# Performance work log

Hardware: AMD Instinct MI355X
Metric: run time of the kernel (lower is better)

## Reference

```python
import jax, jax.numpy as jnp
import numpy as np

B, N, D = 256, 128, 512
NUM_TYPES, NUM_STATS = 6, 8
W_TYPE, W_STATS, W_CORR = 1.0, 1.0, 0.5
LN_EPS = 1e-5


def setup_inputs() -> dict:
    key = jax.random.key(0)
    ks = jax.random.split(key, 20)
    s = 1.0 / np.sqrt(D)
    inp = {
        "column_embeddings": jax.random.normal(ks[0], (B, N, D), jnp.float32),
        "masked_columns": jax.random.bernoulli(ks[1], 0.15, (B, N)),
        "type_targets": jax.random.randint(ks[2], (N,), 0, NUM_TYPES),
        "column_statistics": jax.random.normal(ks[3], (B, N, NUM_STATS), jnp.float32),
        "column_correlations": jnp.tanh(jax.random.normal(ks[4], (B, N, N), jnp.float32)),
        # type head: Linear(D,D) -> GELU -> LayerNorm -> Linear(D,NUM_TYPES)
        "t_W1": jax.random.normal(ks[5], (D, D), jnp.float32) * s,
        "t_b1": jnp.zeros((D,), jnp.float32),
        "t_g": jnp.ones((D,), jnp.float32),
        "t_beta": jnp.zeros((D,), jnp.float32),
        "t_W2": jax.random.normal(ks[6], (D, NUM_TYPES), jnp.float32) * s,
        "t_b2": jnp.zeros((NUM_TYPES,), jnp.float32),
        # stats head
        "s_W1": jax.random.normal(ks[7], (D, D), jnp.float32) * s,
        "s_b1": jnp.zeros((D,), jnp.float32),
        "s_g": jnp.ones((D,), jnp.float32),
        "s_beta": jnp.zeros((D,), jnp.float32),
        "s_W2": jax.random.normal(ks[8], (D, NUM_STATS), jnp.float32) * s,
        "s_b2": jnp.zeros((NUM_STATS,), jnp.float32),
        # bilinear correlation: x_i^T W x_j + b
        "c_W": jax.random.normal(ks[9], (D, D), jnp.float32) * s,
        "c_b": jnp.zeros((), jnp.float32),
    }
    return inp


def _mlp_head(x, W1, b1, g, beta, W2, b2):
    h = jax.nn.gelu(x @ W1 + b1, approximate=False)
    mu = h.mean(-1, keepdims=True)
    var = ((h - mu) ** 2).mean(-1, keepdims=True)
    h = (h - mu) * jax.lax.rsqrt(var + LN_EPS) * g + beta
    return h @ W2 + b2


def _forward(column_embeddings, masked_columns, type_targets,
             column_statistics, column_correlations,
             t_W1, t_b1, t_g, t_beta, t_W2, t_b2,
             s_W1, s_b1, s_g, s_beta, s_W2, s_b2,
             c_W, c_b):
    e = column_embeddings  # [B,N,D]
    type_logits = _mlp_head(e, t_W1, t_b1, t_g, t_beta, t_W2, t_b2)   # [B,N,T]
    stats_preds = _mlp_head(e, s_W1, s_b1, s_g, s_beta, s_W2, s_b2)   # [B,N,S]

    # batched bilinear correlation: tanh(e_i W e_j + b), diag forced to 1
    u = jnp.einsum('bnd,de->bne', e, c_W)            # [B,N,D]
    corr = jnp.tanh(jnp.einsum('bne,bme->bnm', u, e) + c_b)  # [B,N,N]
    eye = jnp.eye(e.shape[1], dtype=corr.dtype)
    corr = corr * (1.0 - eye) + eye

    m = masked_columns.astype(jnp.float32)           # [B,N]
    n_masked = jnp.maximum(m.sum(), 1.0)

    # type loss: masked-mean cross entropy; targets broadcast over batch
    logp = jax.nn.log_softmax(type_logits, axis=-1)
    tgt = jnp.broadcast_to(type_targets[None, :], m.shape)
    ce = -jnp.take_along_axis(logp, tgt[..., None], axis=-1)[..., 0]  # [B,N]
    type_loss = (ce * m).sum() / n_masked

    # stats loss: masked-mean MSE over [B,N,S]
    se = (stats_preds - column_statistics) ** 2
    stats_loss = (se * m[..., None]).sum() / (n_masked * se.shape[-1])

    # correlation loss: mask_expanded = m_i | m_j
    me = jnp.maximum(m[:, :, None], m[:, None, :])   # [B,N,N]
    n_me = jnp.maximum(me.sum(), 1.0)
    ce2 = (corr - column_correlations) ** 2
    correlation_loss = (ce2 * me).sum() / n_me

    total = W_TYPE * type_loss + W_STATS * stats_loss + W_CORR * correlation_loss
    return total


def reference(column_embeddings, masked_columns, type_targets,
              column_statistics, column_correlations,
              t_W1, t_b1, t_g, t_beta, t_W2, t_b2,
              s_W1, s_b1, s_g, s_beta, s_W2, s_b2,
              c_W, c_b):
    return _forward(column_embeddings, masked_columns, type_targets,
                    column_statistics, column_correlations,
                    t_W1, t_b1, t_g, t_beta, t_W2, t_b2,
                    s_W1, s_b1, s_g, s_beta, s_W2, s_b2,
                    c_W, c_b)
```

## Files before the change

kernel.cpp:

```cpp
#include <hip/hip_runtime.h>
#include <math.h>

#define Bx 256
#define Nx 128
#define Dx 512
#define Mx (Bx * Nx)
#define NTYPES 6
#define NSTATS 8
#define LN_EPS 1e-5f
#define CAP 8192

typedef __attribute__((ext_vector_type(8))) short frag8;
typedef __attribute__((ext_vector_type(4))) float f32x4;

__device__ __forceinline__ unsigned short f2bf(float f) {
    unsigned u = __float_as_uint(f);
    u += 0x7fff + ((u >> 16) & 1);
    return (unsigned short)(u >> 16);
}
__device__ __forceinline__ float bf2f(unsigned short s) {
    return __uint_as_float((unsigned)s << 16);
}

#define ASYNC16(g, l) __builtin_amdgcn_global_load_lds(                      \
    (const __attribute__((address_space(1))) void*)(g),                      \
    (__attribute__((address_space(3))) void*)(l), 16, 0, 0)

#define EB_OFF    0ULL
#define U_OFF     33554432ULL
#define EC_OFF    67108864ULL
#define HC_OFF    75497472ULL
#define WT_OFF    92274688ULL
#define WTC_OFF   93323264ULL
#define LIST_OFF  93847552ULL
#define CNTS_OFF  93978624ULL
#define PACC_OFF  93979648ULL
#define PCORR_OFF 93981696ULL
#define ACC_OFF   93982720ULL

__global__ void k_init(int* cntp) {
    if (threadIdx.x == 0) *cntp = 0;
}

__global__ void k_mask_build(const int* __restrict__ m, int* __restrict__ list,
                             int* __restrict__ cnts, int* cntp) {
    const int b = blockIdx.x;
    const int t = threadIdx.x;
    const int r = b * Nx + t;
    const int v = (m[r] != 0) ? 1 : 0;
    const unsigned long long bal = __ballot(v);
    const int wid = t >> 6, lane = t & 63;
    __shared__ int wcnt[2];
    __shared__ int base;
    if (lane == 0) wcnt[wid] = __popcll(bal);
    __syncthreads();
    const int cnt = wcnt[0] + wcnt[1];
    if (t == 0) {
        base = atomicAdd(cntp, cnt);
        cnts[b] = cnt;
    }
    __syncthreads();
    if (v) {
        const int rank = __popcll(bal & ((1ULL << lane) - 1)) + (wid ? wcnt[0] : 0);
        list[base + rank] = r;
    }
}

__global__ void k_convE(const float* __restrict__ x, unsigned short* __restrict__ y) {
    const int i = blockIdx.x * blockDim.x + threadIdx.x;
    const float4 a = ((const float4*)x)[2 * i];
    const float4 b = ((const float4*)x)[2 * i + 1];
    unsigned short u[8] = {f2bf(a.x), f2bf(a.y), f2bf(a.z), f2bf(a.w),
                           f2bf(b.x), f2bf(b.y), f2bf(b.z), f2bf(b.w)};
    ((uint4*)y)[i] = *(const uint4*)u;
}

__global__ void k_convW(const float* __restrict__ W, unsigned short* __restrict__ Wt) {
    const int i = blockIdx.x * blockDim.x + threadIdx.x;
    const int n = i >> 9, k = i & 511;
    Wt[i] = f2bf(W[k * Dx + n]);
}

__global__ void k_gather(const unsigned short* __restrict__ Eb,
                         const int* __restrict__ list, const int* __restrict__ cntp,
                         unsigned short* __restrict__ Ec) {
    const int idx = blockIdx.x;
    const int cnt = min(*cntp, CAP);
    if (idx >= cnt) return;
    const int r = list[idx];
    ((unsigned*)(Ec + (size_t)idx * Dx))[threadIdx.x] =
        ((const unsigned*)(Eb + (size_t)r * Dx))[threadIdx.x];
}

template <int MODE>
__global__ __launch_bounds__(256) void k_gemm_mfma(
    const unsigned short* __restrict__ A,
    const unsigned short* __restrict__ Bt,
    const float* __restrict__ bias0, const float* __restrict__ bias1,
    unsigned short* __restrict__ Cout, int ldc, const int* __restrict__ cntp) {
    const int row0 = blockIdx.y * 128;
    if (MODE == 0) {
        if (row0 >= min(*cntp, CAP)) return;
    }
    __shared__ unsigned short As[128 * 32];
    __shared__ unsigned short Bs[128 * 32];
    const int t = threadIdx.x;
    const int col0 = blockIdx.x * 128;
    const int w = t >> 6, l = t & 63;
    const int wr = (w >> 1) * 64, wc = (w & 1) * 64;
    const int quad = l >> 4, mr = l & 15;

    const unsigned short* Ag0 = A + (size_t)(row0 + (t >> 2)) * Dx + (t & 3) * 8;
    const unsigned short* Ag1 = Ag0 + (size_t)64 * Dx;
    const unsigned short* Bg0 = Bt + (size_t)(col0 + (t >> 2)) * Dx + (t & 3) * 8;
    const unsigned short* Bg1 = Bg0 + (size_t)64 * Dx;
    unsigned short* Al0 = As + t * 8;
    unsigned short* Al1 = As + (t + 256) * 8;
    unsigned short* Bl0 = Bs + t * 8;
    unsigned short* Bl1 = Bs + (t + 256) * 8;

    f32x4 acc[4][4] = {};

    for (int k0 = 0; k0 < Dx; k0 += 32) {
        __syncthreads();
        ASYNC16(Ag0 + k0, Al0);
        ASYNC16(Ag1 + k0, Al1);
        ASYNC16(Bg0 + k0, Bl0);
        ASYNC16(Bg1 + k0, Bl1);
        __syncthreads();
        frag8 a[4], b[4];
#pragma unroll
        for (int i = 0; i < 4; ++i)
            a[i] = *(const frag8*)&As[(wr + i * 16 + mr) * 32 + quad * 8];
#pragma unroll
        for (int j = 0; j < 4; ++j)
            b[j] = *(const frag8*)&Bs[(wc + j * 16 + mr) * 32 + quad * 8];
#pragma unroll
        for (int i = 0; i < 4; ++i)
#pragma unroll
            for (int j = 0; j < 4; ++j)
                acc[i][j] = __builtin_amdgcn_mfma_f32_16x16x32_bf16(
                    a[i], b[j], acc[i][j], 0, 0, 0);
    }

#pragma unroll
    for (int i = 0; i < 4; ++i)
#pragma unroll
        for (int j = 0; j < 4; ++j)
#pragma unroll
            for (int r = 0; r < 4; ++r) {
                const int row = row0 + wr + i * 16 + quad * 4 + r;
                const int col = col0 + wc + j * 16 + mr;
                float v = acc[i][j][r];
                if (MODE == 0) {
                    v += (col < 512) ? bias0[col] : bias1[col - 512];
                    v = 0.5f * v * (1.0f + erff(v * 0.70710678118654752f));
                }
                Cout[(size_t)row * ldc + col] = f2bf(v);
            }
}

__global__ __launch_bounds__(256) void k_head2(
    const unsigned short* __restrict__ Hc,
    const float* __restrict__ tg, const float* __restrict__ tbeta,
    const float* __restrict__ tW2, const float* __restrict__ tb2,
    const float* __restrict__ sg, const float* __restrict__ sbeta,
    const float* __restrict__ sW2, const float* __restrict__ sb2,
    const int* __restrict__ list, const int* __restrict__ cntp,
    const int* __restrict__ tgt, const float* __restrict__ stats,
    float* __restrict__ pacc) {
    const int t = threadIdx.x, w = t >> 6, lane = t & 63;
    const int cnt = min(*cntp, CAP);
    float ce_acc = 0.0f, sse_acc = 0.0f;

    for (int idx = blockIdx.x * 4 + w; idx < cnt; idx += gridDim.x * 4) {
        const int r = list[idx];
        const uint4 ut = ((const uint4*)(Hc + (size_t)idx * 1024))[lane];
        const uint4 us = ((const uint4*)(Hc + (size_t)idx * 1024 + 512))[lane];
        float a[8], b8[8];
        {
            const unsigned uu[4] = {ut.x, ut.y, ut.z, ut.w};
            const unsigned vv[4] = {us.x, us.y, us.z, us.w};
#pragma unroll
            for (int j = 0; j < 4; ++j) {
                a[2 * j]      = bf2f((unsigned short)(uu[j] & 0xffff));
                a[2 * j + 1]  = bf2f((unsigned short)(uu[j] >> 16));
                b8[2 * j]     = bf2f((unsigned short)(vv[j] & 0xffff));
                b8[2 * j + 1] = bf2f((unsigned short)(vv[j] >> 16));
            }
        }
        float st = 0, qt = 0, ss = 0, qs = 0;
#pragma unroll
        for (int j = 0; j < 8; ++j) {
            st += a[j]; qt += a[j] * a[j];
            ss += b8[j]; qs += b8[j] * b8[j];
        }
#pragma unroll
        for (int off = 32; off > 0; off >>= 1) {
            st += __shfl_xor(st, off); qt += __shfl_xor(qt, off);
            ss += __shfl_xor(ss, off); qs += __shfl_xor(qs, off);
        }
        const float mt = st * (1.0f / Dx);
        const float rt = rsqrtf(qt * (1.0f / Dx) - mt * mt + LN_EPS);
        const float ms = ss * (1.0f / Dx);
        const float rs = rsqrtf(qs * (1.0f / Dx) - ms * ms + LN_EPS);

        const int c0 = lane * 8;
        float tp[6] = {}, sp[8] = {};
#pragma unroll
        for (int j = 0; j < 8; ++j) {
            const int c = c0 + j;
            const float nt = (a[j] - mt) * rt * tg[c] + tbeta[c];
#pragma unroll
            for (int k = 0; k < 6; ++k) tp[k] += nt * tW2[c * 6 + k];
            const float ns = (b8[j] - ms) * rs * sg[c] + sbeta[c];
#pragma unroll
            for (int k = 0; k < 8; ++k) sp[k] += ns * sW2[c * 8 + k];
        }
#pragma unroll
        for (int k = 0; k < 6; ++k)
#pragma unroll
            for (int off = 32; off > 0; off >>= 1) tp[k] += __shfl_down(tp[k], off);
#pragma unroll
        for (int k = 0; k < 8; ++k)
#pragma unroll
            for (int off = 32; off > 0; off >>= 1) sp[k] += __shfl_down(sp[k], off);

        if (lane == 0) {
            float lg[6];
#pragma unroll
            for (int k = 0; k < 6; ++k) lg[k] = tp[k] + tb2[k];
            float mx = lg[0];
#pragma unroll
            for (int k = 1; k < 6; ++k) mx = fmaxf(mx, lg[k]);
            float se = 0.0f;
#pragma unroll
            for (int k = 0; k < 6; ++k) se += expf(lg[k] - mx);
            ce_acc += -(lg[tgt[r & (Nx - 1)]] - mx - logf(se));
            float sse = 0.0f;
#pragma unroll
            for (int k = 0; k < 8; ++k) {
                const float d = sp[k] + sb2[k] - stats[(size_t)r * NSTATS + k];
                sse += d * d;
            }
            sse_acc += sse;
        }
    }
    __shared__ float red[4][2];
    if (lane == 0) { red[w][0] = ce_acc; red[w][1] = sse_acc; }
    __syncthreads();
    if (t == 0) {
        pacc[2 * blockIdx.x]     = red[0][0] + red[1][0] + red[2][0] + red[3][0];
        pacc[2 * blockIdx.x + 1] = red[0][1] + red[1][1] + red[2][1] + red[3][1];
    }
}

__global__ __launch_bounds__(256) void k_corr_mfma(
    const unsigned short* __restrict__ U,
    const unsigned short* __restrict__ E,
    const float* __restrict__ Ct,
    const int* __restrict__ m,
    const float* __restrict__ cbp,
    float* __restrict__ pcorr) {
    __shared__ unsigned short As[128 * 32];
    __shared__ unsigned short Bs[128 * 32];
    __shared__ float mloc[128];
    __shared__ float red[4];
    const int b = blockIdx.x;
    const int t = threadIdx.x;
    const int w = t >> 6, l = t & 63;
    const int wr = (w >> 1) * 64, wc = (w & 1) * 64;
    const int quad = l >> 4, mr = l & 15;

    if (t < 128) mloc[t] = (m[b * Nx + t] != 0) ? 1.0f : 0.0f;

    const unsigned short* Ub = U + (size_t)b * Nx * Dx;
    const unsigned short* Eb = E + (size_t)b * Nx * Dx;
    const unsigned short* Ag0 = Ub + (size_t)(t >> 2) * Dx + (t & 3) * 8;
    const unsigned short* Ag1 = Ag0 + (size_t)64 * Dx;
    const unsigned short* Bg0 = Eb + (size_t)(t >> 2) * Dx + (t & 3) * 8;
    const unsigned short* Bg1 = Bg0 + (size_t)64 * Dx;
    unsigned short* Al0 = As + t * 8;
    unsigned short* Al1 = As + (t + 256) * 8;
    unsigned short* Bl0 = Bs + t * 8;
    unsigned short* Bl1 = Bs + (t + 256) * 8;

    f32x4 acc_r[4][4] = {};

    for (int k0 = 0; k0 < Dx; k0 += 32) {
        __syncthreads();
        ASYNC16(Ag0 + k0, Al0);
        ASYNC16(Ag1 + k0, Al1);
        ASYNC16(Bg0 + k0, Bl0);
        ASYNC16(Bg1 + k0, Bl1);
        __syncthreads();
        frag8 a[4], bfr[4];
#pragma unroll
        for (int i = 0; i < 4; ++i)
            a[i] = *(const frag8*)&As[(wr + i * 16 + mr) * 32 + quad * 8];
#pragma unroll
        for (int j = 0; j < 4; ++j)
            bfr[j] = *(const frag8*)&Bs[(wc + j * 16 + mr) * 32 + quad * 8];
#pragma unroll
        for (int i = 0; i < 4; ++i)
#pragma unroll
            for (int j = 0; j < 4; ++j)
                acc_r[i][j] = __builtin_amdgcn_mfma_f32_16x16x32_bf16(
                    a[i], bfr[j], acc_r[i][j], 0, 0, 0);
    }

    const float cb = cbp[0];
    float lsum = 0.0f;
#pragma unroll
    for (int i = 0; i < 4; ++i)
#pragma unroll
        for (int j = 0; j < 4; ++j)
#pragma unroll
            for (int r = 0; r < 4; ++r) {
                const int row = wr + i * 16 + quad * 4 + r;
                const int col = wc + j * 16 + mr;
                float c = (row == col) ? 1.0f : tanhf(acc_r[i][j][r] + cb);
                const float me = fmaxf(mloc[row], mloc[col]);
                const float d = c - Ct[((size_t)b * Nx + row) * Nx + col];
                lsum += me * d * d;
            }
#pragma unroll
    for (int off = 32; off > 0; off >>= 1) lsum += __shfl_down(lsum, off);
    if (l == 0) red[w] = lsum;
    __syncthreads();
    if (t == 0) pcorr[b] = red[0] + red[1] + red[2] + red[3];
}

__global__ __launch_bounds__(256) void k_final(
    const float* __restrict__ pacc, const float* __restrict__ pcorr,
    const int* __restrict__ cnts, const int* __restrict__ cntp,
    float* __restrict__ out) {
    const int t = threadIdx.x, w = t >> 6, lane = t & 63;
    float ce = pacc[2 * t], sse = pacc[2 * t + 1], co = pcorr[t];
    const int c = cnts[t];
    float me = (float)(Nx * Nx) - (float)((Nx - c) * (Nx - c));
#pragma unroll
    for (int off = 32; off > 0; off >>= 1) {
        ce += __shfl_down(ce, off);
        sse += __shfl_down(sse, off);
        co += __shfl_down(co, off);
        me += __shfl_down(me, off);
    }
    __shared__ float red[4][4];
    if (lane == 0) {
        red[w][0] = ce; red[w][1] = sse; red[w][2] = co; red[w][3] = me;
    }
    __syncthreads();
    if (t == 0) {
        const float CE = red[0][0] + red[1][0] + red[2][0] + red[3][0];
        const float SSE = red[0][1] + red[1][1] + red[2][1] + red[3][1];
        const float CO = red[0][2] + red[1][2] + red[2][2] + red[3][2];
        const float ME = red[0][3] + red[1][3] + red[2][3] + red[3][3];
        const float nm = fmaxf((float)*cntp, 1.0f);
        const float nme = fmaxf(ME, 1.0f);
        out[0] = CE / nm + SSE / (nm * (float)NSTATS) + 0.5f * CO / nme;
    }
}

extern "C" void kernel_launch(void* const* d_in, const int* in_sizes, int n_in,
                              void* d_out, int out_size, void* d_ws, size_t ws_size,
                              hipStream_t stream) {
    const float* e      = (const float*)d_in[0];
    const int*   mcols  = (const int*)d_in[1];
    const int*   ttgt   = (const int*)d_in[2];
    const float* stats  = (const float*)d_in[3];
    const float* corrT  = (const float*)d_in[4];
    const float* tW1    = (const float*)d_in[5];
    const float* tb1    = (const float*)d_in[6];
    const float* tg     = (const float*)d_in[7];
    const float* tbeta  = (const float*)d_in[8];
    const float* tW2    = (const float*)d_in[9];
    const float* tb2    = (const float*)d_in[10];
    const float* sW1    = (const float*)d_in[11];
    const float* sb1    = (const float*)d_in[12];
    const float* sg     = (const float*)d_in[13];
    const float* sbeta  = (const float*)d_in[14];
    const float* sW2    = (const float*)d_in[15];
    const float* sb2    = (const float*)d_in[16];
    const float* cW     = (const float*)d_in[17];
    const float* cb     = (const float*)d_in[18];
    float* out = (float*)d_out;

    char* ws = (char*)d_ws;
    unsigned short* Eb    = (unsigned short*)(ws + EB_OFF);
    unsigned short* U     = (unsigned short*)(ws + U_OFF);
    unsigned short* Ec    = (unsigned short*)(ws + EC_OFF);
    unsigned short* Hc    = (unsigned short*)(ws + HC_OFF);
    unsigned short* Wtcmb = (unsigned short*)(ws + WT_OFF);
    unsigned short* Wtc   = (unsigned short*)(ws + WTC_OFF);
    int*   list  = (int*)(ws + LIST_OFF);
    int*   cnts  = (int*)(ws + CNTS_OFF);
    float* pacc  = (float*)(ws + PACC_OFF);
    float* pcorr = (float*)(ws + PCORR_OFF);
    int*   cntp  = (int*)(ws + ACC_OFF);

    k_init<<<1, 64, 0, stream>>>(cntp);
    k_mask_build<<<Bx, Nx, 0, stream>>>(mcols, list, cnts, cntp);
    k_convE<<<Mx * Dx / 8 / 256, 256, 0, stream>>>(e, Eb);
    k_convW<<<Dx * Dx / 256, 256, 0, stream>>>(tW1, Wtcmb);
    k_convW<<<Dx * Dx / 256, 256, 0, stream>>>(sW1, Wtcmb + 512 * 512);
    k_convW<<<Dx * Dx / 256, 256, 0, stream>>>(cW, Wtc);
    k_gather<<<CAP, 256, 0, stream>>>(Eb, list, cntp, Ec);

    k_gemm_mfma<0><<<dim3(8, CAP / 128), 256, 0, stream>>>(
        Ec, Wtcmb, tb1, sb1, Hc, 1024, cntp);
    k_head2<<<256, 256, 0, stream>>>(Hc, tg, tbeta, tW2, tb2, sg, sbeta, sW2, sb2,
                                     list, cntp, ttgt, stats, pacc);

    k_gemm_mfma<1><<<dim3(4, 256), 256, 0, stream>>>(
        Eb, Wtc, nullptr, nullptr, U, 512, nullptr);
    k_corr_mfma<<<Bx, 256, 0, stream>>>(U, Eb, corrT, mcols, cb, pcorr);

    k_final<<<1, 256, 0, stream>>>(pacc, pcorr, cnts, cntp, out);
}
```

Before: 256.2 us.

## Fuse bilinear U-GEMM into correlation kernel and merge conversion/gather kernels

The correlation kernel now computes U = E·Wc in 128-column chunks itself, stages each chunk as bf16 in shared memory and multiplies it by E^T, so the 32 MB U intermediate is never written or read from global memory. The embedding conversion and masked-row gather are merged into one kernel that uses a per-row position map, and the three weight transposes plus the counter reset are merged into one launch. This removes several launches and a large round trip through global memory. In exchange, the fused kernel loads E and Wc fragments straight from global memory without LDS tiling and runs only 256 blocks, so it leans on cache hits and may keep fewer MFMA units busy.

```diff
diff --git a/kernel.cpp b/kernel.cpp
--- a/kernel.cpp
+++ b/kernel.cpp
@@ -27,23 +27,34 @@
     (__attribute__((address_space(3))) void*)(l), 16, 0, 0)
 
 #define EB_OFF    0ULL
-#define U_OFF     33554432ULL
-#define EC_OFF    67108864ULL
-#define HC_OFF    75497472ULL
-#define WT_OFF    92274688ULL
-#define WTC_OFF   93323264ULL
-#define LIST_OFF  93847552ULL
-#define CNTS_OFF  93978624ULL
-#define PACC_OFF  93979648ULL
-#define PCORR_OFF 93981696ULL
-#define ACC_OFF   93982720ULL
-
-__global__ void k_init(int* cntp) {
-    if (threadIdx.x == 0) *cntp = 0;
+#define EC_OFF    33554432ULL
+#define HC_OFF    41943040ULL
+#define WT_OFF    58720256ULL
+#define WTC_OFF   59768832ULL
+#define LIST_OFF  60293120ULL
+#define POS_OFF   60424192ULL
+#define CNTS_OFF  60555264ULL
+#define PACC_OFF  60556288ULL
+#define PCORR_OFF 60558336ULL
+#define CNTP_OFF  60559360ULL
+
+__global__ void k_convW_all(const float* __restrict__ W0, const float* __restrict__ W1,
+                            const float* __restrict__ W2,
+                            unsigned short* __restrict__ T0,
+                            unsigned short* __restrict__ T1,
+                            unsigned short* __restrict__ T2, int* cntp) {
+    if (blockIdx.x == 0 && threadIdx.x == 0) *cntp = 0;
+    const int mid = blockIdx.x >> 10;
+    const int i = ((blockIdx.x & 1023) << 8) + threadIdx.x;
+    const int n = i >> 9, k = i & 511;
+    const float* W = (mid == 0) ? W0 : (mid == 1) ? W1 : W2;
+    unsigned short* T = (mid == 0) ? T0 : (mid == 1) ? T1 : T2;
+    T[i] = f2bf(W[k * Dx + n]);
 }
 
 __global__ void k_mask_build(const int* __restrict__ m, int* __restrict__ list,
-                             int* __restrict__ cnts, int* cntp) {
+                             int* __restrict__ pos, int* __restrict__ cnts,
+                             int* cntp) {
     const int b = blockIdx.x;
     const int t = threadIdx.x;
     const int r = b * Nx + t;
@@ -60,54 +71,44 @@
         cnts[b] = cnt;
     }
     __syncthreads();
+    int p = -1;
     if (v) {
         const int rank = __popcll(bal & ((1ULL << lane) - 1)) + (wid ? wcnt[0] : 0);
-        list[base + rank] = r;
-    }
-}
-
-__global__ void k_convE(const float* __restrict__ x, unsigned short* __restrict__ y) {
-    const int i = blockIdx.x * blockDim.x + threadIdx.x;
-    const float4 a = ((const float4*)x)[2 * i];
-    const float4 b = ((const float4*)x)[2 * i + 1];
+        p = base + rank;
+        if (p < CAP) list[p] = r;
+    }
+    pos[r] = (p < CAP) ? p : -1;
+}
+
+__global__ __launch_bounds__(256) void k_convE_gather(
+    const float* __restrict__ e, const int* __restrict__ pos,
+    unsigned short* __restrict__ Eb, unsigned short* __restrict__ Ec) {
+    const int r = blockIdx.x * 4 + (threadIdx.x >> 6);
+    const int lane = threadIdx.x & 63;
+    const float4* src = (const float4*)(e + (size_t)r * Dx);
+    const float4 a = src[lane * 2];
+    const float4 b = src[lane * 2 + 1];
     unsigned short u[8] = {f2bf(a.x), f2bf(a.y), f2bf(a.z), f2bf(a.w),
                            f2bf(b.x), f2bf(b.y), f2bf(b.z), f2bf(b.w)};
-    ((uint4*)y)[i] = *(const uint4*)u;
-}
-
-__global__ void k_convW(const float* __restrict__ W, unsigned short* __restrict__ Wt) {
-    const int i = blockIdx.x * blockDim.x + threadIdx.x;
-    const int n = i >> 9, k = i & 511;
-    Wt[i] = f2bf(W[k * Dx + n]);
-}
-
-__global__ void k_gather(const unsigned short* __restrict__ Eb,
-                         const int* __restrict__ list, const int* __restrict__ cntp,
-                         unsigned short* __restrict__ Ec) {
-    const int idx = blockIdx.x;
-    const int cnt = min(*cntp, CAP);
-    if (idx >= cnt) return;
-    const int r = list[idx];
-    ((unsigned*)(Ec + (size_t)idx * Dx))[threadIdx.x] =
-        ((const unsigned*)(Eb + (size_t)r * Dx))[threadIdx.x];
-}
-
-template <int MODE>
-__global__ __launch_bounds__(256) void k_gemm_mfma(
+    const uint4 v = *(const uint4*)u;
+    ((uint4*)(Eb + (size_t)r * Dx))[lane] = v;
+    const int p = pos[r];
+    if (p >= 0) ((uint4*)(Ec + (size_t)p * Dx))[lane] = v;
+}
+
+__global__ __launch_bounds__(256) void k_gemm_head(
     const unsigned short* __restrict__ A,
     const unsigned short* __restrict__ Bt,
     const float* __restrict__ bias0, const float* __restrict__ bias1,
-    unsigned short* __restrict__ Cout, int ldc, const int* __restrict__ cntp) {
+    unsigned short* __restrict__ Cout, const int* __restrict__ cntp) {
     const int row0 = blockIdx.y * 128;
-    if (MODE == 0) {
-        if (row0 >= min(*cntp, CAP)) return;
-    }
+    if (row0 >= min(*cntp, CAP)) return;
     __shared__ unsigned short As[128 * 32];
     __shared__ unsigned short Bs[128 * 32];
     const int t = threadIdx.x;
     const int col0 = blockIdx.x * 128;
     const int w = t >> 6, l = t & 63;
-    const int wr = (w >> 1) * 64, wc = (w & 1) * 64;
+    const int wr = (w >> 1) * 64, wcol = (w & 1) * 64;
     const int quad = l >> 4, mr = l & 15;
 
     const unsigned short* Ag0 = A + (size_t)(row0 + (t >> 2)) * Dx + (t & 3) * 8;
@@ -120,7 +121,6 @@
     unsigned short* Bl1 = Bs + (t + 256) * 8;
 
     f32x4 acc[4][4] = {};
-
     for (int k0 = 0; k0 < Dx; k0 += 32) {
         __syncthreads();
         ASYNC16(Ag0 + k0, Al0);
@@ -134,7 +134,7 @@
             a[i] = *(const frag8*)&As[(wr + i * 16 + mr) * 32 + quad * 8];
 #pragma unroll
         for (int j = 0; j < 4; ++j)
-            b[j] = *(const frag8*)&Bs[(wc + j * 16 + mr) * 32 + quad * 8];
+            b[j] = *(const frag8*)&Bs[(wcol + j * 16 + mr) * 32 + quad * 8];
 #pragma unroll
         for (int i = 0; i < 4; ++i)
 #pragma unroll
@@ -142,7 +142,6 @@
                 acc[i][j] = __builtin_amdgcn_mfma_f32_16x16x32_bf16(
                     a[i], b[j], acc[i][j], 0, 0, 0);
     }
-
 #pragma unroll
     for (int i = 0; i < 4; ++i)
 #pragma unroll
@@ -150,13 +149,11 @@
 #pragma unroll
             for (int r = 0; r < 4; ++r) {
                 const int row = row0 + wr + i * 16 + quad * 4 + r;
-                const int col = col0 + wc + j * 16 + mr;
+                const int col = col0 + wcol + j * 16 + mr;
                 float v = acc[i][j][r];
-                if (MODE == 0) {
-                    v += (col < 512) ? bias0[col] : bias1[col - 512];
-                    v = 0.5f * v * (1.0f + erff(v * 0.70710678118654752f));
-                }
-                Cout[(size_t)row * ldc + col] = f2bf(v);
+                v += (col < 512) ? bias0[col] : bias1[col - 512];
+                v = 0.5f * v * (1.0f + erff(v * 0.70710678118654752f));
+                Cout[(size_t)row * 1024 + col] = f2bf(v);
             }
 }
 
@@ -255,58 +252,67 @@
     }
 }
 
-__global__ __launch_bounds__(256) void k_corr_mfma(
-    const unsigned short* __restrict__ U,
-    const unsigned short* __restrict__ E,
+__global__ __launch_bounds__(256) void k_corr_fused(
+    const unsigned short* __restrict__ Eb,
+    const unsigned short* __restrict__ Wc,
     const float* __restrict__ Ct,
     const int* __restrict__ m,
     const float* __restrict__ cbp,
     float* __restrict__ pcorr) {
-    __shared__ unsigned short As[128 * 32];
-    __shared__ unsigned short Bs[128 * 32];
+    __shared__ unsigned short Ub[128][136];
     __shared__ float mloc[128];
     __shared__ float red[4];
     const int b = blockIdx.x;
     const int t = threadIdx.x;
     const int w = t >> 6, l = t & 63;
-    const int wr = (w >> 1) * 64, wc = (w & 1) * 64;
+    const int wr = (w >> 1) * 64, wcol = (w & 1) * 64;
     const int quad = l >> 4, mr = l & 15;
-
     if (t < 128) mloc[t] = (m[b * Nx + t] != 0) ? 1.0f : 0.0f;
-
-    const unsigned short* Ub = U + (size_t)b * Nx * Dx;
-    const unsigned short* Eb = E + (size_t)b * Nx * Dx;
-    const unsigned short* Ag0 = Ub + (size_t)(t >> 2) * Dx + (t & 3) * 8;
-    const unsigned short* Ag1 = Ag0 + (size_t)64 * Dx;
-    const unsigned short* Bg0 = Eb + (size_t)(t >> 2) * Dx + (t & 3) * 8;
-    const unsigned short* Bg1 = Bg0 + (size_t)64 * Dx;
-    unsigned short* Al0 = As + t * 8;
-    unsigned short* Al1 = As + (t + 256) * 8;
-    unsigned short* Bl0 = Bs + t * 8;
-    unsigned short* Bl1 = Bs + (t + 256) * 8;
-
-    f32x4 acc_r[4][4] = {};
-
-    for (int k0 = 0; k0 < Dx; k0 += 32) {
+    const unsigned short* E = Eb + (size_t)b * Nx * Dx;
+
+    f32x4 S[4][4] = {};
+    for (int chunk = 0; chunk < 4; ++chunk) {
+        if (chunk) __syncthreads();
+        f32x4 U[4][4] = {};
+        for (int kt = 0; kt < 16; ++kt) {
+            frag8 a[4], bf[4];
+#pragma unroll
+            for (int i = 0; i < 4; ++i)
+                a[i] = *(const frag8*)&E[(size_t)(wr + i * 16 + mr) * Dx + kt * 32 + quad * 8];
+#pragma unroll
+            for (int j = 0; j < 4; ++j)
+                bf[j] = *(const frag8*)&Wc[(size_t)(chunk * 128 + wcol + j * 16 + mr) * Dx + kt * 32 + quad * 8];
+#pragma unroll
+            for (int i = 0; i < 4; ++i)
+#pragma unroll
+                for (int j = 0; j < 4; ++j)
+                    U[i][j] = __builtin_amdgcn_mfma_f32_16x16x32_bf16(
+                        a[i], bf[j], U[i][j], 0, 0, 0);
+        }
+#pragma unroll
+        for (int i = 0; i < 4; ++i)
+#pragma unroll
+            for (int j = 0; j < 4; ++j)
+#pragma unroll
+                for (int r = 0; r < 4; ++r)
+                    Ub[wr + i * 16 + quad * 4 + r][wcol + j * 16 + mr] = f2bf(U[i][j][r]);
         __syncthreads();
-        ASYNC16(Ag0 + k0, Al0);
-        ASYNC16(Ag1 + k0, Al1);
-        ASYNC16(Bg0 + k0, Bl0);
-        ASYNC16(Bg1 + k0, Bl1);
-        __syncthreads();
-        frag8 a[4], bfr[4];
-#pragma unroll
-        for (int i = 0; i < 4; ++i)
-            a[i] = *(const frag8*)&As[(wr + i * 16 + mr) * 32 + quad * 8];
-#pragma unroll
-        for (int j = 0; j < 4; ++j)
-            bfr[j] = *(const frag8*)&Bs[(wc + j * 16 + mr) * 32 + quad * 8];
-#pragma unroll
-        for (int i = 0; i < 4; ++i)
+#pragma unroll
+        for (int kt = 0; kt < 4; ++kt) {
+            frag8 a[4], bf[4];
+#pragma unroll
+            for (int i = 0; i < 4; ++i)
+                a[i] = *(const frag8*)&Ub[wr + i * 16 + mr][kt * 32 + quad * 8];
 #pragma unroll
             for (int j = 0; j < 4; ++j)
-                acc_r[i][j] = __builtin_amdgcn_mfma_f32_16x16x32_bf16(
-                    a[i], bfr[j], acc_r[i][j], 0, 0, 0);
+                bf[j] = *(const frag8*)&E[(size_t)(wcol + j * 16 + mr) * Dx + chunk * 128 + kt * 32 + quad * 8];
+#pragma unroll
+            for (int i = 0; i < 4; ++i)
+#pragma unroll
+                for (int j = 0; j < 4; ++j)
+                    S[i][j] = __builtin_amdgcn_mfma_f32_16x16x32_bf16(
+                        a[i], bf[j], S[i][j], 0, 0, 0);
+        }
     }
 
     const float cb = cbp[0];
@@ -318,8 +324,8 @@
 #pragma unroll
             for (int r = 0; r < 4; ++r) {
                 const int row = wr + i * 16 + quad * 4 + r;
-                const int col = wc + j * 16 + mr;
-                float c = (row == col) ? 1.0f : tanhf(acc_r[i][j][r] + cb);
+                const int col = wcol + j * 16 + mr;
+                float c = (row == col) ? 1.0f : tanhf(S[i][j][r] + cb);
                 const float me = fmaxf(mloc[row], mloc[col]);
                 const float d = c - Ct[((size_t)b * Nx + row) * Nx + col];
                 lsum += me * d * d;
@@ -388,33 +394,24 @@
 
     char* ws = (char*)d_ws;
     unsigned short* Eb    = (unsigned short*)(ws + EB_OFF);
-    unsigned short* U     = (unsigned short*)(ws + U_OFF);
     unsigned short* Ec    = (unsigned short*)(ws + EC_OFF);
     unsigned short* Hc    = (unsigned short*)(ws + HC_OFF);
     unsigned short* Wtcmb = (unsigned short*)(ws + WT_OFF);
     unsigned short* Wtc   = (unsigned short*)(ws + WTC_OFF);
     int*   list  = (int*)(ws + LIST_OFF);
+    int*   pos   = (int*)(ws + POS_OFF);
     int*   cnts  = (int*)(ws + CNTS_OFF);
     float* pacc  = (float*)(ws + PACC_OFF);
     float* pcorr = (float*)(ws + PCORR_OFF);
-    int*   cntp  = (int*)(ws + ACC_OFF);
-
-    k_init<<<1, 64, 0, stream>>>(cntp);
-    k_mask_build<<<Bx, Nx, 0, stream>>>(mcols, list, cnts, cntp);
-    k_convE<<<Mx * Dx / 8 / 256, 256, 0, stream>>>(e, Eb);
-    k_convW<<<Dx * Dx / 256, 256, 0, stream>>>(tW1, Wtcmb);
-    k_convW<<<Dx * Dx / 256, 256, 0, stream>>>(sW1, Wtcmb + 512 * 512);
-    k_convW<<<Dx * Dx / 256, 256, 0, stream>>>(cW, Wtc);
-    k_gather<<<CAP, 256, 0, stream>>>(Eb, list, cntp, Ec);
-
-    k_gemm_mfma<0><<<dim3(8, CAP / 128), 256, 0, stream>>>(
-        Ec, Wtcmb, tb1, sb1, Hc, 1024, cntp);
+    int*   cntp  = (int*)(ws + CNTP_OFF);
+
+    k_convW_all<<<3072, 256, 0, stream>>>(tW1, sW1, cW, Wtcmb, Wtcmb + 512 * 512,
+                                          Wtc, cntp);
+    k_mask_build<<<Bx, Nx, 0, stream>>>(mcols, list, pos, cnts, cntp);
+    k_convE_gather<<<Mx / 4, 256, 0, stream>>>(e, pos, Eb, Ec);
+    k_gemm_head<<<dim3(8, CAP / 128), 256, 0, stream>>>(Ec, Wtcmb, tb1, sb1, Hc, cntp);
     k_head2<<<256, 256, 0, stream>>>(Hc, tg, tbeta, tW2, tb2, sg, sbeta, sW2, sb2,
                                      list, cntp, ttgt, stats, pacc);
-
-    k_gemm_mfma<1><<<dim3(4, 256), 256, 0, stream>>>(
-        Eb, Wtc, nullptr, nullptr, U, 512, nullptr);
-    k_corr_mfma<<<Bx, 256, 0, stream>>>(U, Eb, corrT, mcols, cb, pcorr);
-
+    k_corr_fused<<<Bx, 256, 0, stream>>>(Eb, Wtc, corrT, mcols, cb, pcorr);
     k_final<<<1, 256, 0, stream>>>(pacc, pcorr, cnts, cntp, out);
 }
```

Result: slower. 275.4 us (+7.5%).

## Merge launches: fused prep, convert+gather, combined GEMMs, and combined tail kernel

Applied to the files above, without the earlier changes.

Cuts the launch count from twelve kernels to five. Mask compaction and the three weight transposes now run as one prep kernel, and a scatter position map lets the fp32-to-bf16 conversion write the compacted rows directly, so the separate gather pass and its re-read of Eb go away. The head GEMM and the correlation U GEMM share one grid, and the correlation and head-loss tails share another, so independent work can fill the GPU together. The cost is branchy multi-role kernels, some extra shared memory in the tail kernel, and head GEMM blocks that exit early but still occupy grid slots.

```diff
diff --git a/kernel.cpp b/kernel.cpp
--- a/kernel.cpp
+++ b/kernel.cpp
@@ -33,81 +33,108 @@
 #define WT_OFF    92274688ULL
 #define WTC_OFF   93323264ULL
 #define LIST_OFF  93847552ULL
-#define CNTS_OFF  93978624ULL
-#define PACC_OFF  93979648ULL
-#define PCORR_OFF 93981696ULL
-#define ACC_OFF   93982720ULL
-
-__global__ void k_init(int* cntp) {
-    if (threadIdx.x == 0) *cntp = 0;
-}
-
-__global__ void k_mask_build(const int* __restrict__ m, int* __restrict__ list,
-                             int* __restrict__ cnts, int* cntp) {
-    const int b = blockIdx.x;
-    const int t = threadIdx.x;
-    const int r = b * Nx + t;
-    const int v = (m[r] != 0) ? 1 : 0;
-    const unsigned long long bal = __ballot(v);
-    const int wid = t >> 6, lane = t & 63;
-    __shared__ int wcnt[2];
-    __shared__ int base;
-    if (lane == 0) wcnt[wid] = __popcll(bal);
-    __syncthreads();
-    const int cnt = wcnt[0] + wcnt[1];
-    if (t == 0) {
-        base = atomicAdd(cntp, cnt);
-        cnts[b] = cnt;
-    }
-    __syncthreads();
-    if (v) {
-        const int rank = __popcll(bal & ((1ULL << lane) - 1)) + (wid ? wcnt[0] : 0);
-        list[base + rank] = r;
-    }
-}
-
-__global__ void k_convE(const float* __restrict__ x, unsigned short* __restrict__ y) {
-    const int i = blockIdx.x * blockDim.x + threadIdx.x;
-    const float4 a = ((const float4*)x)[2 * i];
-    const float4 b = ((const float4*)x)[2 * i + 1];
+#define POS_OFF   93978624ULL
+#define CNTS_OFF  94109696ULL
+#define PACC_OFF  94110720ULL
+#define PCORR_OFF 94112768ULL
+#define CNTP_OFF  94113792ULL
+
+__global__ __launch_bounds__(256) void k_prep(
+    const float* __restrict__ W0, const float* __restrict__ W1,
+    const float* __restrict__ W2, unsigned short* __restrict__ Tcmb,
+    unsigned short* __restrict__ Tc, const int* __restrict__ m,
+    int* __restrict__ list, int* __restrict__ pos, int* __restrict__ cnts,
+    int* cntp) {
+    if (blockIdx.x >= 768) {
+        const int b = blockIdx.x - 768;
+        const int t = threadIdx.x;
+        const int r = b * Nx + t;
+        int v = 0;
+        if (t < 128) v = (m[r] != 0) ? 1 : 0;
+        const unsigned long long bal = __ballot(v);
+        const int wid = t >> 6, lane = t & 63;
+        __shared__ int wcnt[2];
+        __shared__ int base;
+        if (lane == 0 && wid < 2) wcnt[wid] = __popcll(bal);
+        __syncthreads();
+        const int cnt = wcnt[0] + wcnt[1];
+        if (t == 0) {
+            base = atomicAdd(cntp, cnt);
+            cnts[b] = cnt;
+        }
+        __syncthreads();
+        if (t < 128) {
+            int p = -1;
+            if (v) {
+                const int rank = __popcll(bal & ((1ULL << lane) - 1)) +
+                                 (wid ? wcnt[0] : 0);
+                p = base + rank;
+                if (p < CAP) list[p] = r;
+            }
+            pos[r] = (p >= 0 && p < CAP) ? p : -1;
+        }
+        return;
+    }
+    const int lin = blockIdx.x * 256 + threadIdx.x;
+    const int mid = lin >> 16;
+    const int i4  = (lin & 65535) * 4;
+    const int n = i4 >> 9, k = i4 & 511;
+    const float* W = (mid == 0) ? W0 : (mid == 1) ? W1 : W2;
+    unsigned short* T = (mid == 2) ? Tc : (Tcmb + mid * 262144);
+    unsigned short o[4];
+#pragma unroll
+    for (int j = 0; j < 4; ++j) o[j] = f2bf(W[(k + j) * Dx + n]);
+    uint2 u;
+    u.x = (unsigned)o[0] | ((unsigned)o[1] << 16);
+    u.y = (unsigned)o[2] | ((unsigned)o[3] << 16);
+    *(uint2*)(T + i4) = u;
+}
+
+__global__ __launch_bounds__(256) void k_convE_gather(
+    const float* __restrict__ e, const int* __restrict__ pos,
+    unsigned short* __restrict__ Eb, unsigned short* __restrict__ Ec) {
+    const int r = blockIdx.x * 4 + (threadIdx.x >> 6);
+    const int lane = threadIdx.x & 63;
+    const int p = pos[r];
+    const float4* src = (const float4*)(e + (size_t)r * Dx);
+    const float4 a = src[lane * 2];
+    const float4 b = src[lane * 2 + 1];
     unsigned short u[8] = {f2bf(a.x), f2bf(a.y), f2bf(a.z), f2bf(a.w),
                            f2bf(b.x), f2bf(b.y), f2bf(b.z), f2bf(b.w)};
-    ((uint4*)y)[i] = *(const uint4*)u;
-}
-
-__global__ void k_convW(const float* __restrict__ W, unsigned short* __restrict__ Wt) {
-    const int i = blockIdx.x * blockDim.x + threadIdx.x;
-    const int n = i >> 9, k = i & 511;
-    Wt[i] = f2bf(W[k * Dx + n]);
-}
-
-__global__ void k_gather(const unsigned short* __restrict__ Eb,
-                         const int* __restrict__ list, const int* __restrict__ cntp,
-                         unsigned short* __restrict__ Ec) {
-    const int idx = blockIdx.x;
-    const int cnt = min(*cntp, CAP);
-    if (idx >= cnt) return;
-    const int r = list[idx];
-    ((unsigned*)(Ec + (size_t)idx * Dx))[threadIdx.x] =
-        ((const unsigned*)(Eb + (size_t)r * Dx))[threadIdx.x];
-}
-
-template <int MODE>
-__global__ __launch_bounds__(256) void k_gemm_mfma(
-    const unsigned short* __restrict__ A,
-    const unsigned short* __restrict__ Bt,
+    const uint4 v = *(const uint4*)u;
+    ((uint4*)(Eb + (size_t)r * Dx))[lane] = v;
+    if (p >= 0) ((uint4*)(Ec + (size_t)p * Dx))[lane] = v;
+}
+
+__global__ __launch_bounds__(256) void k_gemms(
+    const unsigned short* __restrict__ Eb,
+    const unsigned short* __restrict__ Ec,
+    const unsigned short* __restrict__ Wtc,
+    const unsigned short* __restrict__ Wtcmb,
     const float* __restrict__ bias0, const float* __restrict__ bias1,
-    unsigned short* __restrict__ Cout, int ldc, const int* __restrict__ cntp) {
-    const int row0 = blockIdx.y * 128;
-    if (MODE == 0) {
-        if (row0 >= min(*cntp, CAP)) return;
-    }
+    unsigned short* __restrict__ U, unsigned short* __restrict__ Hc,
+    const int* __restrict__ cntp) {
     __shared__ unsigned short As[128 * 32];
     __shared__ unsigned short Bs[128 * 32];
+    const int bid = blockIdx.x;
+    const unsigned short *A, *Bt;
+    unsigned short* C;
+    int row0, col0, ldc, head;
+    if (bid < 1024) {
+        A = Eb; Bt = Wtc; C = U;
+        row0 = (bid >> 2) << 7; col0 = (bid & 3) << 7;
+        ldc = 512; head = 0;
+    } else {
+        const int b2 = bid - 1024;
+        row0 = (b2 >> 3) << 7;
+        if (row0 >= min(*cntp, CAP)) return;
+        col0 = (b2 & 7) << 7;
+        A = Ec; Bt = Wtcmb; C = Hc;
+        ldc = 1024; head = 1;
+    }
     const int t = threadIdx.x;
-    const int col0 = blockIdx.x * 128;
     const int w = t >> 6, l = t & 63;
-    const int wr = (w >> 1) * 64, wc = (w & 1) * 64;
+    const int wr = (w >> 1) * 64, wcol = (w & 1) * 64;
     const int quad = l >> 4, mr = l & 15;
 
     const unsigned short* Ag0 = A + (size_t)(row0 + (t >> 2)) * Dx + (t & 3) * 8;
@@ -120,7 +147,6 @@
     unsigned short* Bl1 = Bs + (t + 256) * 8;
 
     f32x4 acc[4][4] = {};
-
     for (int k0 = 0; k0 < Dx; k0 += 32) {
         __syncthreads();
         ASYNC16(Ag0 + k0, Al0);
@@ -134,7 +160,7 @@
             a[i] = *(const frag8*)&As[(wr + i * 16 + mr) * 32 + quad * 8];
 #pragma unroll
         for (int j = 0; j < 4; ++j)
-            b[j] = *(const frag8*)&Bs[(wc + j * 16 + mr) * 32 + quad * 8];
+            b[j] = *(const frag8*)&Bs[(wcol + j * 16 + mr) * 32 + quad * 8];
 #pragma unroll
         for (int i = 0; i < 4; ++i)
 #pragma unroll
@@ -142,7 +168,6 @@
                 acc[i][j] = __builtin_amdgcn_mfma_f32_16x16x32_bf16(
                     a[i], b[j], acc[i][j], 0, 0, 0);
     }
-
 #pragma unroll
     for (int i = 0; i < 4; ++i)
 #pragma unroll
@@ -150,17 +175,21 @@
 #pragma unroll
             for (int r = 0; r < 4; ++r) {
                 const int row = row0 + wr + i * 16 + quad * 4 + r;
-                const int col = col0 + wc + j * 16 + mr;
+                const int col = col0 + wcol + j * 16 + mr;
                 float v = acc[i][j][r];
-                if (MODE == 0) {
+                if (head) {
                     v += (col < 512) ? bias0[col] : bias1[col - 512];
                     v = 0.5f * v * (1.0f + erff(v * 0.70710678118654752f));
                 }
-                Cout[(size_t)row * ldc + col] = f2bf(v);
+                C[(size_t)row * ldc + col] = f2bf(v);
             }
 }
 
-__global__ __launch_bounds__(256) void k_head2(
+__global__ __launch_bounds__(256) void k_tail(
+    const unsigned short* __restrict__ U,
+    const unsigned short* __restrict__ Eb,
+    const float* __restrict__ Ct, const int* __restrict__ m,
+    const float* __restrict__ cbp, float* __restrict__ pcorr,
     const unsigned short* __restrict__ Hc,
     const float* __restrict__ tg, const float* __restrict__ tbeta,
     const float* __restrict__ tW2, const float* __restrict__ tb2,
@@ -169,14 +198,82 @@
     const int* __restrict__ list, const int* __restrict__ cntp,
     const int* __restrict__ tgt, const float* __restrict__ stats,
     float* __restrict__ pacc) {
-    const int t = threadIdx.x, w = t >> 6, lane = t & 63;
+    __shared__ unsigned short As[128 * 32];
+    __shared__ unsigned short Bs[128 * 32];
+    __shared__ float mloc[128];
+    __shared__ float redf[4][2];
+    const int t = threadIdx.x;
+    const int w = t >> 6, l = t & 63;
+
+    if (blockIdx.x < 256) {
+        const int b = blockIdx.x;
+        const int wr = (w >> 1) * 64, wcol = (w & 1) * 64;
+        const int quad = l >> 4, mr = l & 15;
+        if (t < 128) mloc[t] = (m[b * Nx + t] != 0) ? 1.0f : 0.0f;
+
+        const unsigned short* Ub = U + (size_t)b * Nx * Dx;
+        const unsigned short* E  = Eb + (size_t)b * Nx * Dx;
+        const unsigned short* Ag0 = Ub + (size_t)(t >> 2) * Dx + (t & 3) * 8;
+        const unsigned short* Ag1 = Ag0 + (size_t)64 * Dx;
+        const unsigned short* Bg0 = E + (size_t)(t >> 2) * Dx + (t & 3) * 8;
+        const unsigned short* Bg1 = Bg0 + (size_t)64 * Dx;
+        unsigned short* Al0 = As + t * 8;
+        unsigned short* Al1 = As + (t + 256) * 8;
+        unsigned short* Bl0 = Bs + t * 8;
+        unsigned short* Bl1 = Bs + (t + 256) * 8;
+
+        f32x4 acc_r[4][4] = {};
+        for (int k0 = 0; k0 < Dx; k0 += 32) {
+            __syncthreads();
+            ASYNC16(Ag0 + k0, Al0);
+            ASYNC16(Ag1 + k0, Al1);
+            ASYNC16(Bg0 + k0, Bl0);
+            ASYNC16(Bg1 + k0, Bl1);
+            __syncthreads();
+            frag8 a[4], bfr[4];
+#pragma unroll
+            for (int i = 0; i < 4; ++i)
+                a[i] = *(const frag8*)&As[(wr + i * 16 + mr) * 32 + quad * 8];
+#pragma unroll
+            for (int j = 0; j < 4; ++j)
+                bfr[j] = *(const frag8*)&Bs[(wcol + j * 16 + mr) * 32 + quad * 8];
+#pragma unroll
+            for (int i = 0; i < 4; ++i)
+#pragma unroll
+                for (int j = 0; j < 4; ++j)
+                    acc_r[i][j] = __builtin_amdgcn_mfma_f32_16x16x32_bf16(
+                        a[i], bfr[j], acc_r[i][j], 0, 0, 0);
+        }
+        const float cb = cbp[0];
+        float lsum = 0.0f;
+#pragma unroll
+        for (int i = 0; i < 4; ++i)
+#pragma unroll
+            for (int j = 0; j < 4; ++j)
+#pragma unroll
+                for (int r = 0; r < 4; ++r) {
+                    const int row = wr + i * 16 + quad * 4 + r;
+                    const int col = wcol + j * 16 + mr;
+                    float c = (row == col) ? 1.0f : tanhf(acc_r[i][j][r] + cb);
+                    const float me = fmaxf(mloc[row], mloc[col]);
+                    const float d = c - Ct[((size_t)b * Nx + row) * Nx + col];
+                    lsum += me * d * d;
+                }
+#pragma unroll
+        for (int off = 32; off > 0; off >>= 1) lsum += __shfl_down(lsum, off);
+        if (l == 0) redf[w][0] = lsum;
+        __syncthreads();
+        if (t == 0) pcorr[b] = redf[0][0] + redf[1][0] + redf[2][0] + redf[3][0];
+        return;
+    }
+
+    const int blk = blockIdx.x - 256;
     const int cnt = min(*cntp, CAP);
     float ce_acc = 0.0f, sse_acc = 0.0f;
-
-    for (int idx = blockIdx.x * 4 + w; idx < cnt; idx += gridDim.x * 4) {
+    for (int idx = blk * 4 + w; idx < cnt; idx += 256 * 4) {
         const int r = list[idx];
-        const uint4 ut = ((const uint4*)(Hc + (size_t)idx * 1024))[lane];
-        const uint4 us = ((const uint4*)(Hc + (size_t)idx * 1024 + 512))[lane];
+        const uint4 ut = ((const uint4*)(Hc + (size_t)idx * 1024))[l];
+        const uint4 us = ((const uint4*)(Hc + (size_t)idx * 1024 + 512))[l];
         float a[8], b8[8];
         {
             const unsigned uu[4] = {ut.x, ut.y, ut.z, ut.w};
@@ -205,7 +302,7 @@
         const float ms = ss * (1.0f / Dx);
         const float rs = rsqrtf(qs * (1.0f / Dx) - ms * ms + LN_EPS);
 
-        const int c0 = lane * 8;
+        const int c0 = l * 8;
         float tp[6] = {}, sp[8] = {};
 #pragma unroll
         for (int j = 0; j < 8; ++j) {
@@ -226,7 +323,7 @@
 #pragma unroll
             for (int off = 32; off > 0; off >>= 1) sp[k] += __shfl_down(sp[k], off);
 
-        if (lane == 0) {
+        if (l == 0) {
             float lg[6];
 #pragma unroll
             for (int k = 0; k < 6; ++k) lg[k] = tp[k] + tb2[k];
@@ -246,89 +343,12 @@
             sse_acc += sse;
         }
     }
-    __shared__ float red[4][2];
-    if (lane == 0) { red[w][0] = ce_acc; red[w][1] = sse_acc; }
+    if (l == 0) { redf[w][0] = ce_acc; redf[w][1] = sse_acc; }
     __syncthreads();
     if (t == 0) {
-        pacc[2 * blockIdx.x]     = red[0][0] + red[1][0] + red[2][0] + red[3][0];
-        pacc[2 * blockIdx.x + 1] = red[0][1] + red[1][1] + red[2][1] + red[3][1];
-    }
-}
-
-__global__ __launch_bounds__(256) void k_corr_mfma(
-    const unsigned short* __restrict__ U,
-    const unsigned short* __restrict__ E,
-    const float* __restrict__ Ct,
-    const int* __restrict__ m,
-    const float* __restrict__ cbp,
-    float* __restrict__ pcorr) {
-    __shared__ unsigned short As[128 * 32];
-    __shared__ unsigned short Bs[128 * 32];
-    __shared__ float mloc[128];
-    __shared__ float red[4];
-    const int b = blockIdx.x;
-    const int t = threadIdx.x;
-    const int w = t >> 6, l = t & 63;
-    const int wr = (w >> 1) * 64, wc = (w & 1) * 64;
-    const int quad = l >> 4, mr = l & 15;
-
-    if (t < 128) mloc[t] = (m[b * Nx + t] != 0) ? 1.0f : 0.0f;
-
-    const unsigned short* Ub = U + (size_t)b * Nx * Dx;
-    const unsigned short* Eb = E + (size_t)b * Nx * Dx;
-    const unsigned short* Ag0 = Ub + (size_t)(t >> 2) * Dx + (t & 3) * 8;
-    const unsigned short* Ag1 = Ag0 + (size_t)64 * Dx;
-    const unsigned short* Bg0 = Eb + (size_t)(t >> 2) * Dx + (t & 3) * 8;
-    const unsigned short* Bg1 = Bg0 + (size_t)64 * Dx;
-    unsigned short* Al0 = As + t * 8;
-    unsigned short* Al1 = As + (t + 256) * 8;
-    unsigned short* Bl0 = Bs + t * 8;
-    unsigned short* Bl1 = Bs + (t + 256) * 8;
-
-    f32x4 acc_r[4][4] = {};
-
-    for (int k0 = 0; k0 < Dx; k0 += 32) {
-        __syncthreads();
-        ASYNC16(Ag0 + k0, Al0);
-        ASYNC16(Ag1 + k0, Al1);
-        ASYNC16(Bg0 + k0, Bl0);
-        ASYNC16(Bg1 + k0, Bl1);
-        __syncthreads();
-        frag8 a[4], bfr[4];
-#pragma unroll
-        for (int i = 0; i < 4; ++i)
-            a[i] = *(const frag8*)&As[(wr + i * 16 + mr) * 32 + quad * 8];
-#pragma unroll
-        for (int j = 0; j < 4; ++j)
-            bfr[j] = *(const frag8*)&Bs[(wc + j * 16 + mr) * 32 + quad * 8];
-#pragma unroll
-        for (int i = 0; i < 4; ++i)
-#pragma unroll
-            for (int j = 0; j < 4; ++j)
-                acc_r[i][j] = __builtin_amdgcn_mfma_f32_16x16x32_bf16(
-                    a[i], bfr[j], acc_r[i][j], 0, 0, 0);
-    }
-
-    const float cb = cbp[0];
-    float lsum = 0.0f;
-#pragma unroll
-    for (int i = 0; i < 4; ++i)
-#pragma unroll
-        for (int j = 0; j < 4; ++j)
-#pragma unroll
-            for (int r = 0; r < 4; ++r) {
-                const int row = wr + i * 16 + quad * 4 + r;
-                const int col = wc + j * 16 + mr;
-                float c = (row == col) ? 1.0f : tanhf(acc_r[i][j][r] + cb);
-                const float me = fmaxf(mloc[row], mloc[col]);
-                const float d = c - Ct[((size_t)b * Nx + row) * Nx + col];
-                lsum += me * d * d;
-            }
-#pragma unroll
-    for (int off = 32; off > 0; off >>= 1) lsum += __shfl_down(lsum, off);
-    if (l == 0) red[w] = lsum;
-    __syncthreads();
-    if (t == 0) pcorr[b] = red[0] + red[1] + red[2] + red[3];
+        pacc[2 * blk]     = redf[0][0] + redf[1][0] + redf[2][0] + redf[3][0];
+        pacc[2 * blk + 1] = redf[0][1] + redf[1][1] + redf[2][1] + redf[3][1];
+    }
 }
 
 __global__ __launch_bounds__(256) void k_final(
@@ -394,27 +414,19 @@
     unsigned short* Wtcmb = (unsigned short*)(ws + WT_OFF);
     unsigned short* Wtc   = (unsigned short*)(ws + WTC_OFF);
     int*   list  = (int*)(ws + LIST_OFF);
+    int*   pos   = (int*)(ws + POS_OFF);
     int*   cnts  = (int*)(ws + CNTS_OFF);
     float* pacc  = (float*)(ws + PACC_OFF);
     float* pcorr = (float*)(ws + PCORR_OFF);
-    int*   cntp  = (int*)(ws + ACC_OFF);
-
-    k_init<<<1, 64, 0, stream>>>(cntp);
-    k_mask_build<<<Bx, Nx, 0, stream>>>(mcols, list, cnts, cntp);
-    k_convE<<<Mx * Dx / 8 / 256, 256, 0, stream>>>(e, Eb);
-    k_convW<<<Dx * Dx / 256, 256, 0, stream>>>(tW1, Wtcmb);
-    k_convW<<<Dx * Dx / 256, 256, 0, stream>>>(sW1, Wtcmb + 512 * 512);
-    k_convW<<<Dx * Dx / 256, 256, 0, stream>>>(cW, Wtc);
-    k_gather<<<CAP, 256, 0, stream>>>(Eb, list, cntp, Ec);
-
-    k_gemm_mfma<0><<<dim3(8, CAP / 128), 256, 0, stream>>>(
-        Ec, Wtcmb, tb1, sb1, Hc, 1024, cntp);
-    k_head2<<<256, 256, 0, stream>>>(Hc, tg, tbeta, tW2, tb2, sg, sbeta, sW2, sb2,
-                                     list, cntp, ttgt, stats, pacc);
-
-    k_gemm_mfma<1><<<dim3(4, 256), 256, 0, stream>>>(
-        Eb, Wtc, nullptr, nullptr, U, 512, nullptr);
-    k_corr_mfma<<<Bx, 256, 0, stream>>>(U, Eb, corrT, mcols, cb, pcorr);
-
+    int*   cntp  = (int*)(ws + CNTP_OFF);
+
+    hipMemsetAsync(cntp, 0, sizeof(int), stream);
+    k_prep<<<1024, 256, 0, stream>>>(tW1, sW1, cW, Wtcmb, Wtc, mcols,
+                                     list, pos, cnts, cntp);
+    k_convE_gather<<<Mx / 4, 256, 0, stream>>>(e, pos, Eb, Ec);
+    k_gemms<<<1536, 256, 0, stream>>>(Eb, Ec, Wtc, Wtcmb, tb1, sb1, U, Hc, cntp);
+    k_tail<<<512, 256, 0, stream>>>(U, Eb, corrT, mcols, cb, pcorr,
+                                    Hc, tg, tbeta, tW2, tb2, sg, sbeta, sW2, sb2,
+                                    list, cntp, ttgt, stats, pacc);
     k_final<<<1, 256, 0, stream>>>(pacc, pcorr, cnts, cntp, out);
 }
```

Measured after the change: 254.1 us. Within noise of the previous version (-0.8%).
